# Kernel tuning notes

Hardware: AMD Instinct MI355X
Metric: run time of the kernel (lower is better)

## Reference

```python
import jax, jax.numpy as jnp
import numpy as np

N_BLOCK = 3; EMBED = 256; N_HEAD = 8; HEAD = EMBED // N_HEAD
N_AGENT = 8; SEQ = 256; BATCH = 64; ACT_DIM = 32
DECAY_SCALE = 1.0
EPS = 1e-6


def _decay_matrix():
    # Per-head decay kappas as in Mava Sable, decay over timesteps (pos // n_agent), causal mask.
    gammas = (1.0 - jnp.exp(jnp.linspace(jnp.log(1.0 / 32.0), jnp.log(1.0 / 512.0), N_HEAD))) * DECAY_SCALE
    t = (jnp.arange(SEQ) // N_AGENT).astype(jnp.float32)
    diff = t[:, None] - t[None, :]
    causal = jnp.arange(SEQ)[:, None] >= jnp.arange(SEQ)[None, :]
    return jnp.where(causal[None], gammas[:, None, None] ** diff[None], 0.0)  # [H,S,S]


def rmsnorm(x, scale):
    return x * jax.lax.rsqrt(jnp.mean(x * x, -1, keepdims=True) + EPS) * scale


def groupnorm(x, scale, bias):
    # GroupNorm with n_head groups over the feature dim, per position.
    B, S, E = x.shape
    xg = x.reshape(B, S, N_HEAD, HEAD)
    mu = xg.mean(-1, keepdims=True)
    var = ((xg - mu) ** 2).mean(-1, keepdims=True)
    xn = ((xg - mu) * jax.lax.rsqrt(var + 1e-5)).reshape(B, S, E)
    return xn * scale + bias


def retention(q_in, k_in, v_in, wq, wk, wv, wg, wo, gns, gnb, decay):
    # Parallel multi-scale retention: (Q K^T * D) V, groupnorm, swish gate from query input.
    B, S, E = q_in.shape
    q = (q_in @ wq).reshape(B, S, N_HEAD, HEAD).transpose(0, 2, 1, 3)
    k = (k_in @ wk).reshape(B, S, N_HEAD, HEAD).transpose(0, 2, 1, 3) / jnp.sqrt(jnp.float32(HEAD))
    v = (v_in @ wv).reshape(B, S, N_HEAD, HEAD).transpose(0, 2, 1, 3)
    scores = jnp.einsum('bhnd,bhmd->bhnm', q, k) * decay[None]
    ret = jnp.einsum('bhnm,bhmd->bhnd', scores, v)
    ret = groupnorm(ret.transpose(0, 2, 1, 3).reshape(B, S, E), gns, gnb)
    return (jax.nn.swish(q_in @ wg) * ret) @ wo


def swiglu(x, wg, w1, w2):
    return (jax.nn.swish(x @ wg) * (x @ w1)) @ w2


def forward(action, obs_rep, w_enc, ln0, wq1, wk1, wv1, wg1, wo1, gns1, gnb1, ln1,
            wq2, wk2, wv2, wg2, wo2, gns2, gnb2, ln2, swg, sw1, sw2, ln3,
            hw1, hb1, hln, hw2, hb2):
    decay = _decay_matrix()
    x = rmsnorm(jax.nn.gelu(action @ w_enc), ln0)
    for b in range(N_BLOCK):
        r1 = retention(x, x, x, wq1[b], wk1[b], wv1[b], wg1[b], wo1[b], gns1[b], gnb1[b], decay)
        x = rmsnorm(x + r1, ln1[b])
        r2 = retention(obs_rep, x, x, wq2[b], wk2[b], wv2[b], wg2[b], wo2[b], gns2[b], gnb2[b], decay)
        x = rmsnorm(obs_rep + r2, ln2[b])
        x = rmsnorm(x + swiglu(x, swg[b], sw1[b], sw2[b]), ln3[b])
    h = rmsnorm(jax.nn.gelu(x @ hw1 + hb1), hln)
    return h @ hw2 + hb2


def setup_inputs() -> dict:
    key = jax.random.key(0)
    ks = jax.random.split(key, 24)
    E, A, NB = EMBED, ACT_DIM, N_BLOCK
    s = 0.02
    return {
        'action': jax.random.uniform(ks[0], (BATCH, SEQ, A), jnp.float32),
        'obs_rep': jax.random.normal(ks[1], (BATCH, SEQ, E), jnp.float32),
        'w_enc': jax.random.normal(ks[2], (A, E), jnp.float32) * s,
        'ln0': jnp.ones((E,), jnp.float32),
        'wq1': jax.random.normal(ks[3], (NB, E, E), jnp.float32) * s,
        'wk1': jax.random.normal(ks[4], (NB, E, E), jnp.float32) * s,
        'wv1': jax.random.normal(ks[5], (NB, E, E), jnp.float32) * s,
        'wg1': jax.random.normal(ks[6], (NB, E, E), jnp.float32) * s,
        'wo1': jax.random.normal(ks[7], (NB, E, E), jnp.float32) * s,
        'gns1': jnp.ones((NB, E), jnp.float32),
        'gnb1': jnp.zeros((NB, E), jnp.float32),
        'ln1': jnp.ones((NB, E), jnp.float32),
        'wq2': jax.random.normal(ks[8], (NB, E, E), jnp.float32) * s,
        'wk2': jax.random.normal(ks[9], (NB, E, E), jnp.float32) * s,
        'wv2': jax.random.normal(ks[10], (NB, E, E), jnp.float32) * s,
        'wg2': jax.random.normal(ks[11], (NB, E, E), jnp.float32) * s,
        'wo2': jax.random.normal(ks[12], (NB, E, E), jnp.float32) * s,
        'gns2': jnp.ones((NB, E), jnp.float32),
        'gnb2': jnp.zeros((NB, E), jnp.float32),
        'ln2': jnp.ones((NB, E), jnp.float32),
        'swg': jax.random.normal(ks[13], (NB, E, E), jnp.float32) * s,
        'sw1': jax.random.normal(ks[14], (NB, E, E), jnp.float32) * s,
        'sw2': jax.random.normal(ks[15], (NB, E, E), jnp.float32) * s,
        'ln3': jnp.ones((NB, E), jnp.float32),
        'hw1': jax.random.normal(ks[16], (E, E), jnp.float32) * s,
        'hb1': jnp.zeros((E,), jnp.float32),
        'hln': jnp.ones((E,), jnp.float32),
        'hw2': jax.random.normal(ks[17], (E, A), jnp.float32) * s,
        'hb2': jnp.zeros((A,), jnp.float32),
    }


def reference(action, obs_rep, w_enc, ln0, wq1, wk1, wv1, wg1, wo1, gns1, gnb1, ln1,
              wq2, wk2, wv2, wg2, wo2, gns2, gnb2, ln2, swg, sw1, sw2, ln3,
              hw1, hb1, hln, hw2, hb2):
    return forward(action, obs_rep, w_enc, ln0, wq1, wk1, wv1, wg1, wo1, gns1, gnb1, ln1,
                   wq2, wk2, wv2, wg2, wo2, gns2, gnb2, ln2, swg, sw1, sw2, ln3,
                   hw1, hb1, hln, hw2, hb2)
```

## Files before the change

### kernel.cpp

```cpp
#include <hip/hip_runtime.h>
#include <cstdint>
#include <cmath>

typedef __attribute__((ext_vector_type(8))) short short8;
typedef __attribute__((ext_vector_type(4))) float floatx4;

#define DEV static __device__ __forceinline__

DEV float bf2f(uint16_t u) {
    union { uint32_t i; float f; } v; v.i = ((uint32_t)u) << 16; return v.f;
}
DEV uint16_t f2bf(float f) {
    union { float f; uint32_t i; } v; v.f = f;
    uint32_t r = (v.i + 0x7FFFu + ((v.i >> 16) & 1u)) >> 16;
    return (uint16_t)r;
}
DEV float swishf(float x) { return x / (1.f + __expf(-x)); }
DEV float geluf(float x) {
    const float c = 0.7978845608028654f;
    float t = tanhf(c * (x + 0.044715f * x * x * x));
    return 0.5f * x * (1.f + t);
}

#define CHUNK_E 8192
#define MAT_E   65536


struct TArg { const float* src[15]; };

__global__ __launch_bounds__(256) void tpose_k(TArg ta, uint16_t* __restrict__ arena) {
    int z = blockIdx.z;
    const float* src; uint16_t* dst;
    if (z == 0) {
        if (blockIdx.y) return;
        src = ta.src[0]; dst = arena;
    } else if (z <= 39) {
        int q = z - 1; int ti = q / 3, s = q % 3;
        src = ta.src[1 + ti] + (size_t)s * 65536;
        dst = arena + CHUNK_E + (size_t)(ti * 3 + s) * MAT_E;
    } else {
        src = ta.src[14]; dst = arena + CHUNK_E + (size_t)39 * MAT_E;
    }
    int k0 = blockIdx.y << 5;
    int n0 = blockIdx.x << 6;
    __shared__ __align__(16) uint16_t tile[32][72];
    int t = threadIdx.x;
    {
        int r = t >> 3, c = (t & 7) << 3;
        const float* s0 = src + (size_t)(k0 + r) * 256 + n0 + c;
        float4 f0 = *(const float4*)s0;
        float4 f1 = *(const float4*)(s0 + 4);
        tile[r][c + 0] = f2bf(f0.x); tile[r][c + 1] = f2bf(f0.y);
        tile[r][c + 2] = f2bf(f0.z); tile[r][c + 3] = f2bf(f0.w);
        tile[r][c + 4] = f2bf(f1.x); tile[r][c + 5] = f2bf(f1.y);
        tile[r][c + 6] = f2bf(f1.z); tile[r][c + 7] = f2bf(f1.w);
    }
    __syncthreads();
    {
        int n = t >> 2, c = (t & 3) << 3;
        uint16_t tmp[8];
#pragma unroll
        for (int j = 0; j < 8; ++j) tmp[j] = tile[c + j][n];
        *(uint4*)&dst[(size_t)(k0 >> 5) * CHUNK_E + (size_t)(n0 + n) * 32 + c] = *(uint4*)tmp;
    }
}

struct SegArgs {
    const float* action; const float* obs;
    uint16_t *actb, *obsb, *xb, *bq, *bk, *bv, *bg, *brg;
    const float *ln0, *hb1, *hln, *hw2, *hb2;
    float* outp;
    float l2g[8];
};

enum { EP_NONE = 0, EP_GELU_RMS = 1, EP_RESID_RMS = 2 };
enum { EP2_NONE = 0, EP2_SWIGLU = 1 };

template<int EPI, int K>
DEV void gemm_dev(int m0, const uint16_t* __restrict__ A, const uint16_t* __restrict__ Wt,
                  uint16_t* __restrict__ O, const float* __restrict__ bias,
                  const uint16_t* __restrict__ resid, const float* __restrict__ lnw,
                  float (&rowsum)[4][32])
{
    const int t = threadIdx.x;
    const int w = t >> 6, lane = t & 63, l16 = lane & 15, lg = lane >> 4;
    constexpr int NC = K / 32;

    floatx4 acc[2][4];
#pragma unroll
    for (int i = 0; i < 2; ++i)
#pragma unroll
        for (int j = 0; j < 4; ++j) acc[i][j] = (floatx4){0.f, 0.f, 0.f, 0.f};

#pragma unroll
    for (int kc = 0; kc < NC; ++kc) {
        short8 aF[2], bF[4];
#pragma unroll
        for (int rt = 0; rt < 2; ++rt)
            aF[rt] = *(const short8*)(A + (size_t)(m0 + (rt << 4) + l16) * K +
                                      (kc << 5) + (lg << 3));
#pragma unroll
        for (int ct = 0; ct < 4; ++ct)
            bF[ct] = *(const short8*)(Wt + (size_t)kc * CHUNK_E +
                                      (size_t)((w << 6) + (ct << 4) + l16) * 32 + (lg << 3));
#pragma unroll
        for (int rt = 0; rt < 2; ++rt)
#pragma unroll
            for (int ct = 0; ct < 4; ++ct)
                acc[rt][ct] = __builtin_amdgcn_mfma_f32_16x16x32_bf16(
                    aF[rt], bF[ct], acc[rt][ct], 0, 0, 0);
    }

    float v[2][4][4];
#pragma unroll
    for (int rt = 0; rt < 2; ++rt)
#pragma unroll
        for (int ct = 0; ct < 4; ++ct)
#pragma unroll
            for (int r = 0; r < 4; ++r) {
                int row = (rt << 4) + (lg << 2) + r;
                int col = (w << 6) + (ct << 4) + l16;
                size_t idx = (size_t)(m0 + row) * 256 + col;
                float x = acc[rt][ct][r];
                if (EPI == EP_GELU_RMS) { if (bias) x += bias[col]; x = geluf(x); }
                if (EPI == EP_RESID_RMS) x += bf2f(resid[idx]);
                v[rt][ct][r] = x;
            }

    if (EPI == EP_GELU_RMS || EPI == EP_RESID_RMS) {
#pragma unroll
        for (int rt = 0; rt < 2; ++rt)
#pragma unroll
            for (int r = 0; r < 4; ++r) {
                float p = 0.f;
#pragma unroll
                for (int ct = 0; ct < 4; ++ct) p += v[rt][ct][r] * v[rt][ct][r];
                p += __shfl_xor(p, 1, 64); p += __shfl_xor(p, 2, 64);
                p += __shfl_xor(p, 4, 64); p += __shfl_xor(p, 8, 64);
                int row = (rt << 4) + (lg << 2) + r;
                if (l16 == 0) rowsum[w][row] = p;
            }
        __syncthreads();
#pragma unroll
        for (int rt = 0; rt < 2; ++rt)
#pragma unroll
            for (int r = 0; r < 4; ++r) {
                int row = (rt << 4) + (lg << 2) + r;
                float tot = rowsum[0][row] + rowsum[1][row] + rowsum[2][row] + rowsum[3][row];
                float rn = rsqrtf(tot * (1.f / 256.f) + 1e-6f);
#pragma unroll
                for (int ct = 0; ct < 4; ++ct) {
                    int col = (w << 6) + (ct << 4) + l16;
                    size_t idx = (size_t)(m0 + row) * 256 + col;
                    O[idx] = f2bf(v[rt][ct][r] * rn * lnw[col]);
                }
            }
        __syncthreads();
    } else {
#pragma unroll
        for (int rt = 0; rt < 2; ++rt)
#pragma unroll
            for (int ct = 0; ct < 4; ++ct)
#pragma unroll
                for (int r = 0; r < 4; ++r) {
                    int row = (rt << 4) + (lg << 2) + r;
                    int col = (w << 6) + (ct << 4) + l16;
                    O[(size_t)(m0 + row) * 256 + col] = f2bf(v[rt][ct][r]);
                }
    }
}

template<int EPI>
DEV void gemm2_dev(int m0, const uint16_t* __restrict__ A,
                   const uint16_t* __restrict__ W1, const uint16_t* __restrict__ W2,
                   uint16_t* __restrict__ O1, uint16_t* __restrict__ O2)
{
    const int t = threadIdx.x;
    const int w = t >> 6, lane = t & 63, l16 = lane & 15, lg = lane >> 4;

    floatx4 a1[2][4], a2[2][4];
#pragma unroll
    for (int i = 0; i < 2; ++i)
#pragma unroll
        for (int j = 0; j < 4; ++j) {
            a1[i][j] = (floatx4){0.f, 0.f, 0.f, 0.f};
            a2[i][j] = (floatx4){0.f, 0.f, 0.f, 0.f};
        }

#pragma unroll
    for (int kc = 0; kc < 8; ++kc) {
        short8 aF[2], b1[4], b2[4];
#pragma unroll
        for (int rt = 0; rt < 2; ++rt)
            aF[rt] = *(const short8*)(A + (size_t)(m0 + (rt << 4) + l16) * 256 +
                                      (kc << 5) + (lg << 3));
        size_t woff = (size_t)kc * CHUNK_E + (size_t)((w << 6) + l16) * 32 + (lg << 3);
#pragma unroll
        for (int ct = 0; ct < 4; ++ct) {
            b1[ct] = *(const short8*)(W1 + woff + (size_t)(ct << 4) * 32);
            b2[ct] = *(const short8*)(W2 + woff + (size_t)(ct << 4) * 32);
        }
#pragma unroll
        for (int rt = 0; rt < 2; ++rt)
#pragma unroll
            for (int ct = 0; ct < 4; ++ct) {
                a1[rt][ct] = __builtin_amdgcn_mfma_f32_16x16x32_bf16(aF[rt], b1[ct], a1[rt][ct], 0, 0, 0);
                a2[rt][ct] = __builtin_amdgcn_mfma_f32_16x16x32_bf16(aF[rt], b2[ct], a2[rt][ct], 0, 0, 0);
            }
    }

#pragma unroll
    for (int rt = 0; rt < 2; ++rt)
#pragma unroll
        for (int ct = 0; ct < 4; ++ct)
#pragma unroll
            for (int r = 0; r < 4; ++r) {
                int row = (rt << 4) + (lg << 2) + r;
                int col = (w << 6) + (ct << 4) + l16;
                size_t idx = (size_t)(m0 + row) * 256 + col;
                if (EPI == EP2_NONE) {
                    O1[idx] = f2bf(a1[rt][ct][r]);
                    O2[idx] = f2bf(a2[rt][ct][r]);
                } else {
                    O1[idx] = f2bf(swishf(a1[rt][ct][r]) * a2[rt][ct][r]);
                }
            }
}

DEV int rowbase(int blk) { return (blk & 63) * 256 + (blk >> 6) * 32; }


__global__ __launch_bounds__(256, 2) void seg0_k(SegArgs sa, const uint16_t* __restrict__ wenc,
                                                 const uint16_t* __restrict__ wq,
                                                 const uint16_t* __restrict__ wk,
                                                 const uint16_t* __restrict__ wv,
                                                 const uint16_t* __restrict__ wg)
{
    __shared__ float rowsum[4][32];
    const int t = threadIdx.x;
    const int m0 = rowbase(blockIdx.x);
    {
        int r = t >> 3, c = (t & 7) << 2;
        float4 f = *(const float4*)(sa.action + (size_t)(m0 + r) * 32 + c);
        uint16_t tmp[4] = { f2bf(f.x), f2bf(f.y), f2bf(f.z), f2bf(f.w) };
        *(uint2*)(sa.actb + (size_t)(m0 + r) * 32 + c) = *(uint2*)tmp;
    }
    {
        const float4* ob = (const float4*)sa.obs + (size_t)m0 * 64;
        uint2* od = (uint2*)sa.obsb + (size_t)m0 * 64;
#pragma unroll
        for (int j = 0; j < 8; ++j) {
            float4 f = ob[j * 256 + t];
            uint16_t tmp[4] = { f2bf(f.x), f2bf(f.y), f2bf(f.z), f2bf(f.w) };
            od[j * 256 + t] = *(uint2*)tmp;
        }
    }
    __syncthreads();
    gemm_dev<EP_GELU_RMS, 32>(m0, sa.actb, wenc, sa.xb, nullptr, nullptr, sa.ln0, rowsum);
    gemm2_dev<EP2_NONE>(m0, sa.xb, wq, wk, sa.bq, sa.bk);
    gemm2_dev<EP2_NONE>(m0, sa.xb, wv, wg, sa.bv, sa.bg);
}

__global__ __launch_bounds__(256, 2) void attn_k(SegArgs sa, const float* __restrict__ gns,
                                                 const float* __restrict__ gnb)
{
    __shared__ __align__(16) uint16_t QS[256][40];
    __shared__ __align__(16) uint16_t Ks[256][40];
    __shared__ __align__(16) uint16_t Vt[32][264];
    const int b = blockIdx.x & 63, h = blockIdx.x >> 6;
    const float l2g = sa.l2g[h];
    const int t = threadIdx.x, w = t >> 6, lane = t & 63, l16 = lane & 15, lg = lane >> 4;
    const size_t base = ((size_t)b * 256) * 256 + (size_t)h * 32;
    const uint16_t *q = sa.bq, *kbuf = sa.bk, *vbuf = sa.bv, *g = sa.bg;
    uint16_t* out = sa.brg;

    {
        const uint4* qr = (const uint4*)(q + base + (size_t)t * 256);
        *(uint4*)&QS[t][0] = qr[0]; *(uint4*)&QS[t][8] = qr[1];
        *(uint4*)&QS[t][16] = qr[2]; *(uint4*)&QS[t][24] = qr[3];
        const uint4* kr = (const uint4*)(kbuf + base + (size_t)t * 256);
        *(uint4*)&Ks[t][0] = kr[0]; *(uint4*)&Ks[t][8] = kr[1];
        *(uint4*)&Ks[t][16] = kr[2]; *(uint4*)&Ks[t][24] = kr[3];
        union { uint4 v4[4]; uint16_t u[32]; } vv;
        const uint4* vr = (const uint4*)(vbuf + base + (size_t)t * 256);
        vv.v4[0] = vr[0]; vv.v4[1] = vr[1]; vv.v4[2] = vr[2]; vv.v4[3] = vr[3];
#pragma unroll
        for (int d = 0; d < 32; ++d) Vt[d][t] = vv.u[d];
    }
    __syncthreads();

    short8 qF[4];
#pragma unroll
    for (int rt = 0; rt < 4; ++rt)
        qF[rt] = *(const short8*)&QS[(w << 6) + (rt << 4) + l16][lg << 3];

    floatx4 racc[4][2];
#pragma unroll
    for (int i = 0; i < 4; ++i) { racc[i][0] = (floatx4){0,0,0,0}; racc[i][1] = (floatx4){0,0,0,0}; }

    const float invsq = 0.17677669529663687f;
    const int jtmax = 2 * w + 1;
    for (int jt = 0; jt <= jtmax; ++jt) {
        const int j0 = jt << 5;
        floatx4 sacc[4][2];
#pragma unroll
        for (int i = 0; i < 4; ++i) { sacc[i][0] = (floatx4){0,0,0,0}; sacc[i][1] = (floatx4){0,0,0,0}; }
        short8 kF[2];
#pragma unroll
        for (int ct = 0; ct < 2; ++ct)
            kF[ct] = *(const short8*)&Ks[j0 + (ct << 4) + l16][lg << 3];
#pragma unroll
        for (int rt = 0; rt < 4; ++rt)
#pragma unroll
            for (int ct = 0; ct < 2; ++ct)
                sacc[rt][ct] = __builtin_amdgcn_mfma_f32_16x16x32_bf16(
                    qF[rt], kF[ct], sacc[rt][ct], 0, 0, 0);
#pragma unroll
        for (int rt = 0; rt < 4; ++rt)
#pragma unroll
            for (int ct = 0; ct < 2; ++ct)
#pragma unroll
                for (int r = 0; r < 4; ++r) {
                    int row = (rt << 4) + (lg << 2) + r;
                    int i = (w << 6) + row;
                    int j = j0 + (ct << 4) + l16;
                    float svv = 0.f;
                    if (i >= j)
                        svv = sacc[rt][ct][r] * invsq *
                              exp2f((float)((i >> 3) - (j >> 3)) * l2g);
                    QS[(w << 6) + row][(ct << 4) + l16] = f2bf(svv);
                }
        short8 vF[2];
#pragma unroll
        for (int ct = 0; ct < 2; ++ct)
            vF[ct] = *(const short8*)&Vt[(ct << 4) + l16][j0 + (lg << 3)];
#pragma unroll
        for (int rt = 0; rt < 4; ++rt) {
            short8 sF = *(const short8*)&QS[(w << 6) + (rt << 4) + l16][lg << 3];
#pragma unroll
            for (int ct = 0; ct < 2; ++ct)
                racc[rt][ct] = __builtin_amdgcn_mfma_f32_16x16x32_bf16(
                    sF, vF[ct], racc[rt][ct], 0, 0, 0);
        }
    }

#pragma unroll
    for (int rt = 0; rt < 4; ++rt)
#pragma unroll
        for (int r = 0; r < 4; ++r) {
            float v0 = racc[rt][0][r], v1 = racc[rt][1][r];
            float s1 = v0 + v1, s2 = v0 * v0 + v1 * v1;
            s1 += __shfl_xor(s1, 1, 64); s2 += __shfl_xor(s2, 1, 64);
            s1 += __shfl_xor(s1, 2, 64); s2 += __shfl_xor(s2, 2, 64);
            s1 += __shfl_xor(s1, 4, 64); s2 += __shfl_xor(s2, 4, 64);
            s1 += __shfl_xor(s1, 8, 64); s2 += __shfl_xor(s2, 8, 64);
            float mu = s1 * (1.f / 32.f);
            float var = s2 * (1.f / 32.f) - mu * mu;
            float rstd = rsqrtf(var + 1e-5f);
            int srow = (w << 6) + (rt << 4) + (lg << 2) + r;
            size_t obase = ((size_t)b * 256 + srow) * 256 + (size_t)h * 32;
#pragma unroll
            for (int ct = 0; ct < 2; ++ct) {
                int d = (ct << 4) + l16;
                float x = ct ? v1 : v0;
                float y = (x - mu) * rstd * gns[h * 32 + d] + gnb[h * 32 + d];
                float gv = swishf(bf2f(g[obase + d]));
                out[obase + d] = f2bf(y * gv);
            }
        }
}

__global__ __launch_bounds__(256, 2) void g1_k(SegArgs sa,
    const uint16_t* __restrict__ wo, const float* __restrict__ ln1,
    const uint16_t* __restrict__ wq, const uint16_t* __restrict__ wk,
    const uint16_t* __restrict__ wv, const uint16_t* __restrict__ wg)
{
    __shared__ float rowsum[4][32];
    const int m0 = rowbase(blockIdx.x);
    gemm_dev<EP_RESID_RMS, 256>(m0, sa.brg, wo, sa.xb, nullptr, sa.xb, ln1, rowsum);
    gemm2_dev<EP2_NONE>(m0, sa.xb,   wk, wv, sa.bk, sa.bv);
    gemm2_dev<EP2_NONE>(m0, sa.obsb, wq, wg, sa.bq, sa.bg);
}

__global__ __launch_bounds__(256, 2) void g2_k(SegArgs sa,
    const uint16_t* __restrict__ wo, const float* __restrict__ ln2,
    const uint16_t* __restrict__ wswg, const uint16_t* __restrict__ wsw1,
    const uint16_t* __restrict__ wsw2, const float* __restrict__ ln3,
    const uint16_t* __restrict__ nwq, const uint16_t* __restrict__ nwk,
    const uint16_t* __restrict__ nwv, const uint16_t* __restrict__ nwg)
{
    __shared__ float rowsum[4][32];
    const int m0 = rowbase(blockIdx.x);
    gemm_dev<EP_RESID_RMS, 256>(m0, sa.brg, wo, sa.xb, nullptr, sa.obsb, ln2, rowsum);
    gemm2_dev<EP2_SWIGLU>(m0, sa.xb, wswg, wsw1, sa.bk, nullptr);
    __syncthreads();
    gemm_dev<EP_RESID_RMS, 256>(m0, sa.bk, wsw2, sa.xb, nullptr, sa.xb, ln3, rowsum);
    if (nwq) {
        gemm2_dev<EP2_NONE>(m0, sa.xb, nwq, nwk, sa.bq, sa.bk);
        gemm2_dev<EP2_NONE>(m0, sa.xb, nwv, nwg, sa.bv, sa.bg);
    }
}

__global__ __launch_bounds__(256, 2) void head_k(SegArgs sa, const uint16_t* __restrict__ hw1t)
{
    __shared__ float rowsum[4][32];
    __shared__ float w2s[8192];
    const int t = threadIdx.x;
    const int m0 = rowbase(blockIdx.x);
    gemm_dev<EP_GELU_RMS, 256>(m0, sa.xb, hw1t, sa.bq, sa.hb1, nullptr, sa.hln, rowsum);
    __syncthreads();
#pragma unroll
    for (int j = 0; j < 32; ++j) w2s[j * 256 + t] = sa.hw2[j * 256 + t];
    __syncthreads();
    {
        int n = t & 31, rs = t >> 5;
#pragma unroll
        for (int rr = 0; rr < 4; ++rr) {
            int row = m0 + (rr << 3) + rs;
            float a0 = sa.hb2[n];
#pragma unroll 8
            for (int kk = 0; kk < 256; ++kk)
                a0 += bf2f(sa.bq[(size_t)row * 256 + kk]) * w2s[kk * 32 + n];
            sa.outp[(size_t)row * 32 + n] = a0;
        }
    }
}

extern "C" void kernel_launch(void* const* d_in, const int* in_sizes, int n_in,
                              void* d_out, int out_size, void* d_ws, size_t ws_size,
                              hipStream_t stream)
{
    const float* action = (const float*)d_in[0];
    const float* obs    = (const float*)d_in[1];
    const float* w_enc  = (const float*)d_in[2];
    const float* ln0    = (const float*)d_in[3];
    const float* wq1 = (const float*)d_in[4];
    const float* wk1 = (const float*)d_in[5];
    const float* wv1 = (const float*)d_in[6];
    const float* wg1 = (const float*)d_in[7];
    const float* wo1 = (const float*)d_in[8];
    const float* gns1 = (const float*)d_in[9];
    const float* gnb1 = (const float*)d_in[10];
    const float* ln1  = (const float*)d_in[11];
    const float* wq2 = (const float*)d_in[12];
    const float* wk2 = (const float*)d_in[13];
    const float* wv2 = (const float*)d_in[14];
    const float* wg2 = (const float*)d_in[15];
    const float* wo2 = (const float*)d_in[16];
    const float* gns2 = (const float*)d_in[17];
    const float* gnb2 = (const float*)d_in[18];
    const float* ln2  = (const float*)d_in[19];
    const float* swgp = (const float*)d_in[20];
    const float* sw1p = (const float*)d_in[21];
    const float* sw2p = (const float*)d_in[22];
    const float* ln3  = (const float*)d_in[23];
    const float* hw1  = (const float*)d_in[24];
    const float* hb1  = (const float*)d_in[25];
    const float* hln  = (const float*)d_in[26];
    const float* hw2  = (const float*)d_in[27];
    const float* hb2  = (const float*)d_in[28];

    char* ws = (char*)d_ws;
    uint16_t* wt   = (uint16_t*)(ws + 0);
    uint16_t* actb = (uint16_t*)(ws + 6291456);
    uint16_t* obsb = (uint16_t*)(ws + 7340032);
    uint16_t* xb   = (uint16_t*)(ws + 15728640);
    uint16_t* bq   = (uint16_t*)(ws + 24117248);
    uint16_t* bk   = (uint16_t*)(ws + 32505856);
    uint16_t* bv   = (uint16_t*)(ws + 40894464);
    uint16_t* bg   = (uint16_t*)(ws + 49283072);
    uint16_t* brg  = (uint16_t*)(ws + 57671680);

    uint16_t* wtenc = wt;
    uint16_t* hw1t  = wt + CHUNK_E + (size_t)39 * MAT_E;
    auto WTp = [&](int ti, int s) { return wt + CHUNK_E + (size_t)(ti * 3 + s) * MAT_E; };

    TArg ta;
    ta.src[0] = w_enc;
    ta.src[1] = wq1;  ta.src[2] = wk1;  ta.src[3] = wv1;  ta.src[4] = wg1;  ta.src[5] = wo1;
    ta.src[6] = wq2;  ta.src[7] = wk2;  ta.src[8] = wv2;  ta.src[9] = wg2;  ta.src[10] = wo2;
    ta.src[11] = swgp; ta.src[12] = sw1p; ta.src[13] = sw2p; ta.src[14] = hw1;
    tpose_k<<<dim3(4, 8, 41), 256, 0, stream>>>(ta, wt);

    SegArgs sa;
    sa.action = action; sa.obs = obs;
    sa.actb = actb; sa.obsb = obsb; sa.xb = xb;
    sa.bq = bq; sa.bk = bk; sa.bv = bv; sa.bg = bg; sa.brg = brg;
    sa.ln0 = ln0; sa.hb1 = hb1; sa.hln = hln; sa.hw2 = hw2; sa.hb2 = hb2;
    sa.outp = (float*)d_out;
    {
        const double a = log(1.0 / 32.0), bb = log(1.0 / 512.0);
        for (int hh = 0; hh < 8; ++hh) {
            double lg = a + (bb - a) * hh / 7.0;
            double gam = 1.0 - exp(lg);
            sa.l2g[hh] = (float)(log(gam) / log(2.0));
        }
    }

    dim3 GB(512), TB(256);
    seg0_k<<<GB, TB, 0, stream>>>(sa, wtenc, WTp(0, 0), WTp(1, 0), WTp(2, 0), WTp(3, 0));
    for (int b3 = 0; b3 < 3; ++b3) {
        attn_k<<<GB, TB, 0, stream>>>(sa, gns1 + b3 * 256, gnb1 + b3 * 256);
        g1_k<<<GB, TB, 0, stream>>>(sa, WTp(4, b3), ln1 + b3 * 256,
                                    WTp(5, b3), WTp(6, b3), WTp(7, b3), WTp(8, b3));
        attn_k<<<GB, TB, 0, stream>>>(sa, gns2 + b3 * 256, gnb2 + b3 * 256);
        g2_k<<<GB, TB, 0, stream>>>(sa, WTp(9, b3), ln2 + b3 * 256,
                                    WTp(10, b3), WTp(11, b3), WTp(12, b3), ln3 + b3 * 256,
                                    b3 < 2 ? WTp(0, b3 + 1) : nullptr,
                                    b3 < 2 ? WTp(1, b3 + 1) : nullptr,
                                    b3 < 2 ? WTp(2, b3 + 1) : nullptr,
                                    b3 < 2 ? WTp(3, b3 + 1) : nullptr);
    }
    head_k<<<GB, TB, 0, stream>>>(sa, hw1t);
}
```

Baseline: 605.8 us.

## Keep intermediate row tiles in padded LDS between chained GEMMs

The fused GEMM helpers gain template options to read A from, and write outputs to, padded shared-memory tiles (row stride 264). Intermediates produced and consumed by the same block now stay in LDS rather than round-tripping through global bf16 buffers. This covers the encoder output, the post-wo residual norm, the SwiGLU hidden and the head hidden. Global stores are kept only where later kernels need them. The cost is more shared memory per block, which may reduce occupancy below the two blocks per CU that the launch bounds target, especially in g2_k and head_k.

```diff
diff --git a/kernel.cpp b/kernel.cpp
--- a/kernel.cpp
+++ b/kernel.cpp
@@ -24,6 +24,7 @@
 
 #define CHUNK_E 8192
 #define MAT_E   65536
+#define APAD    264
 
 
 struct TArg { const float* src[15]; };
@@ -76,11 +77,17 @@
 enum { EP_NONE = 0, EP_GELU_RMS = 1, EP_RESID_RMS = 2 };
 enum { EP2_NONE = 0, EP2_SWIGLU = 1 };
 
-template<int EPI, int K>
-DEV void gemm_dev(int m0, const uint16_t* __restrict__ A, const uint16_t* __restrict__ Wt,
-                  uint16_t* __restrict__ O, const float* __restrict__ bias,
-                  const uint16_t* __restrict__ resid, const float* __restrict__ lnw,
-                  float (&rowsum)[4][32])
+template<int EPI, int K, int LDA, bool OG, int LDO, bool RL>
+DEV void gemm_u(int m0,
+                const uint16_t* __restrict__ A,
+                const uint16_t* __restrict__ Wt,
+                uint16_t* __restrict__ Og,
+                uint16_t* __restrict__ Ol,
+                const float* __restrict__ bias,
+                const uint16_t* __restrict__ Rg,
+                const uint16_t* __restrict__ Rl,
+                const float* __restrict__ lnw,
+                float (&rowsum)[4][32])
 {
     const int t = threadIdx.x;
     const int w = t >> 6, lane = t & 63, l16 = lane & 15, lg = lane >> 4;
@@ -96,9 +103,13 @@
     for (int kc = 0; kc < NC; ++kc) {
         short8 aF[2], bF[4];
 #pragma unroll
-        for (int rt = 0; rt < 2; ++rt)
-            aF[rt] = *(const short8*)(A + (size_t)(m0 + (rt << 4) + l16) * K +
-                                      (kc << 5) + (lg << 3));
+        for (int rt = 0; rt < 2; ++rt) {
+            int row = (rt << 4) + l16;
+            if constexpr (LDA != 0)
+                aF[rt] = *(const short8*)(A + (size_t)row * LDA + (kc << 5) + (lg << 3));
+            else
+                aF[rt] = *(const short8*)(A + (size_t)(m0 + row) * K + (kc << 5) + (lg << 3));
+        }
 #pragma unroll
         for (int ct = 0; ct < 4; ++ct)
             bF[ct] = *(const short8*)(Wt + (size_t)kc * CHUNK_E +
@@ -120,14 +131,19 @@
             for (int r = 0; r < 4; ++r) {
                 int row = (rt << 4) + (lg << 2) + r;
                 int col = (w << 6) + (ct << 4) + l16;
-                size_t idx = (size_t)(m0 + row) * 256 + col;
                 float x = acc[rt][ct][r];
-                if (EPI == EP_GELU_RMS) { if (bias) x += bias[col]; x = geluf(x); }
-                if (EPI == EP_RESID_RMS) x += bf2f(resid[idx]);
+                if constexpr (EPI == EP_GELU_RMS) {
+                    if (bias) x += bias[col];
+                    x = geluf(x);
+                }
+                if constexpr (EPI == EP_RESID_RMS) {
+                    if constexpr (RL) x += bf2f(Rl[(size_t)row * APAD + col]);
+                    else              x += bf2f(Rg[(size_t)(m0 + row) * 256 + col]);
+                }
                 v[rt][ct][r] = x;
             }
 
-    if (EPI == EP_GELU_RMS || EPI == EP_RESID_RMS) {
+    if constexpr (EPI == EP_GELU_RMS || EPI == EP_RESID_RMS) {
 #pragma unroll
         for (int rt = 0; rt < 2; ++rt)
 #pragma unroll
@@ -151,8 +167,11 @@
 #pragma unroll
                 for (int ct = 0; ct < 4; ++ct) {
                     int col = (w << 6) + (ct << 4) + l16;
-                    size_t idx = (size_t)(m0 + row) * 256 + col;
-                    O[idx] = f2bf(v[rt][ct][r] * rn * lnw[col]);
+                    uint16_t bb = f2bf(v[rt][ct][r] * rn * lnw[col]);
+                    if constexpr (OG)
+                        Og[(size_t)(m0 + row) * 256 + col] = bb;
+                    if constexpr (LDO != 0)
+                        Ol[(size_t)row * LDO + col] = bb;
                 }
             }
         __syncthreads();
@@ -165,15 +184,20 @@
                 for (int r = 0; r < 4; ++r) {
                     int row = (rt << 4) + (lg << 2) + r;
                     int col = (w << 6) + (ct << 4) + l16;
-                    O[(size_t)(m0 + row) * 256 + col] = f2bf(v[rt][ct][r]);
+                    uint16_t bb = f2bf(v[rt][ct][r]);
+                    if constexpr (OG)
+                        Og[(size_t)(m0 + row) * 256 + col] = bb;
+                    if constexpr (LDO != 0)
+                        Ol[(size_t)row * LDO + col] = bb;
                 }
     }
 }
 
-template<int EPI>
-DEV void gemm2_dev(int m0, const uint16_t* __restrict__ A,
-                   const uint16_t* __restrict__ W1, const uint16_t* __restrict__ W2,
-                   uint16_t* __restrict__ O1, uint16_t* __restrict__ O2)
+template<int EPI, int LDA>
+DEV void gemm2_u(int m0, const uint16_t* __restrict__ A,
+                 const uint16_t* __restrict__ W1, const uint16_t* __restrict__ W2,
+                 uint16_t* __restrict__ O1, uint16_t* __restrict__ O2,
+                 uint16_t* __restrict__ Ol)
 {
     const int t = threadIdx.x;
     const int w = t >> 6, lane = t & 63, l16 = lane & 15, lg = lane >> 4;
@@ -191,9 +215,13 @@
     for (int kc = 0; kc < 8; ++kc) {
         short8 aF[2], b1[4], b2[4];
 #pragma unroll
-        for (int rt = 0; rt < 2; ++rt)
-            aF[rt] = *(const short8*)(A + (size_t)(m0 + (rt << 4) + l16) * 256 +
-                                      (kc << 5) + (lg << 3));
+        for (int rt = 0; rt < 2; ++rt) {
+            int row = (rt << 4) + l16;
+            if constexpr (LDA != 0)
+                aF[rt] = *(const short8*)(A + (size_t)row * LDA + (kc << 5) + (lg << 3));
+            else
+                aF[rt] = *(const short8*)(A + (size_t)(m0 + row) * 256 + (kc << 5) + (lg << 3));
+        }
         size_t woff = (size_t)kc * CHUNK_E + (size_t)((w << 6) + l16) * 32 + (lg << 3);
 #pragma unroll
         for (int ct = 0; ct < 4; ++ct) {
@@ -217,12 +245,12 @@
             for (int r = 0; r < 4; ++r) {
                 int row = (rt << 4) + (lg << 2) + r;
                 int col = (w << 6) + (ct << 4) + l16;
-                size_t idx = (size_t)(m0 + row) * 256 + col;
-                if (EPI == EP2_NONE) {
+                if constexpr (EPI == EP2_NONE) {
+                    size_t idx = (size_t)(m0 + row) * 256 + col;
                     O1[idx] = f2bf(a1[rt][ct][r]);
                     O2[idx] = f2bf(a2[rt][ct][r]);
                 } else {
-                    O1[idx] = f2bf(swishf(a1[rt][ct][r]) * a2[rt][ct][r]);
+                    Ol[(size_t)row * APAD + col] = f2bf(swishf(a1[rt][ct][r]) * a2[rt][ct][r]);
                 }
             }
 }
@@ -237,13 +265,15 @@
                                                  const uint16_t* __restrict__ wg)
 {
     __shared__ float rowsum[4][32];
+    __shared__ __align__(16) uint16_t actS[32][40];
+    __shared__ __align__(16) uint16_t T0[32][APAD];
     const int t = threadIdx.x;
     const int m0 = rowbase(blockIdx.x);
     {
         int r = t >> 3, c = (t & 7) << 2;
         float4 f = *(const float4*)(sa.action + (size_t)(m0 + r) * 32 + c);
         uint16_t tmp[4] = { f2bf(f.x), f2bf(f.y), f2bf(f.z), f2bf(f.w) };
-        *(uint2*)(sa.actb + (size_t)(m0 + r) * 32 + c) = *(uint2*)tmp;
+        *(uint2*)&actS[r][c] = *(uint2*)tmp;
     }
     {
         const float4* ob = (const float4*)sa.obs + (size_t)m0 * 64;
@@ -256,9 +286,10 @@
         }
     }
     __syncthreads();
-    gemm_dev<EP_GELU_RMS, 32>(m0, sa.actb, wenc, sa.xb, nullptr, nullptr, sa.ln0, rowsum);
-    gemm2_dev<EP2_NONE>(m0, sa.xb, wq, wk, sa.bq, sa.bk);
-    gemm2_dev<EP2_NONE>(m0, sa.xb, wv, wg, sa.bv, sa.bg);
+    gemm_u<EP_GELU_RMS, 32, 40, true, APAD, false>(m0, &actS[0][0], wenc,
+        sa.xb, &T0[0][0], nullptr, nullptr, nullptr, sa.ln0, rowsum);
+    gemm2_u<EP2_NONE, APAD>(m0, &T0[0][0], wq, wk, sa.bq, sa.bk, nullptr);
+    gemm2_u<EP2_NONE, APAD>(m0, &T0[0][0], wv, wg, sa.bv, sa.bg, nullptr);
 }
 
 __global__ __launch_bounds__(256, 2) void attn_k(SegArgs sa, const float* __restrict__ gns,
@@ -376,10 +407,12 @@
     const uint16_t* __restrict__ wv, const uint16_t* __restrict__ wg)
 {
     __shared__ float rowsum[4][32];
+    __shared__ __align__(16) uint16_t T0[32][APAD];
     const int m0 = rowbase(blockIdx.x);
-    gemm_dev<EP_RESID_RMS, 256>(m0, sa.brg, wo, sa.xb, nullptr, sa.xb, ln1, rowsum);
-    gemm2_dev<EP2_NONE>(m0, sa.xb,   wk, wv, sa.bk, sa.bv);
-    gemm2_dev<EP2_NONE>(m0, sa.obsb, wq, wg, sa.bq, sa.bg);
+    gemm_u<EP_RESID_RMS, 256, 0, false, APAD, false>(m0, sa.brg, wo,
+        nullptr, &T0[0][0], nullptr, sa.xb, nullptr, ln1, rowsum);
+    gemm2_u<EP2_NONE, APAD>(m0, &T0[0][0], wk, wv, sa.bk, sa.bv, nullptr);
+    gemm2_u<EP2_NONE, 0>(m0, sa.obsb, wq, wg, sa.bq, sa.bg, nullptr);
 }
 
 __global__ __launch_bounds__(256, 2) void g2_k(SegArgs sa,
@@ -390,14 +423,18 @@
     const uint16_t* __restrict__ nwv, const uint16_t* __restrict__ nwg)
 {
     __shared__ float rowsum[4][32];
+    __shared__ __align__(16) uint16_t T0[32][APAD];
+    __shared__ __align__(16) uint16_t T1[32][APAD];
     const int m0 = rowbase(blockIdx.x);
-    gemm_dev<EP_RESID_RMS, 256>(m0, sa.brg, wo, sa.xb, nullptr, sa.obsb, ln2, rowsum);
-    gemm2_dev<EP2_SWIGLU>(m0, sa.xb, wswg, wsw1, sa.bk, nullptr);
+    gemm_u<EP_RESID_RMS, 256, 0, false, APAD, false>(m0, sa.brg, wo,
+        nullptr, &T0[0][0], nullptr, sa.obsb, nullptr, ln2, rowsum);
+    gemm2_u<EP2_SWIGLU, APAD>(m0, &T0[0][0], wswg, wsw1, nullptr, nullptr, &T1[0][0]);
     __syncthreads();
-    gemm_dev<EP_RESID_RMS, 256>(m0, sa.bk, wsw2, sa.xb, nullptr, sa.xb, ln3, rowsum);
+    gemm_u<EP_RESID_RMS, 256, APAD, true, APAD, true>(m0, &T1[0][0], wsw2,
+        sa.xb, &T0[0][0], nullptr, nullptr, &T0[0][0], ln3, rowsum);
     if (nwq) {
-        gemm2_dev<EP2_NONE>(m0, sa.xb, nwq, nwk, sa.bq, sa.bk);
-        gemm2_dev<EP2_NONE>(m0, sa.xb, nwv, nwg, sa.bv, sa.bg);
+        gemm2_u<EP2_NONE, APAD>(m0, &T0[0][0], nwq, nwk, sa.bq, sa.bk, nullptr);
+        gemm2_u<EP2_NONE, APAD>(m0, &T0[0][0], nwv, nwg, sa.bv, sa.bg, nullptr);
     }
 }
 
@@ -405,23 +442,23 @@
 {
     __shared__ float rowsum[4][32];
     __shared__ float w2s[8192];
+    __shared__ __align__(16) uint16_t T0[32][APAD];
     const int t = threadIdx.x;
     const int m0 = rowbase(blockIdx.x);
-    gemm_dev<EP_GELU_RMS, 256>(m0, sa.xb, hw1t, sa.bq, sa.hb1, nullptr, sa.hln, rowsum);
-    __syncthreads();
 #pragma unroll
     for (int j = 0; j < 32; ++j) w2s[j * 256 + t] = sa.hw2[j * 256 + t];
-    __syncthreads();
+    gemm_u<EP_GELU_RMS, 256, 0, false, APAD, false>(m0, sa.xb, hw1t,
+        nullptr, &T0[0][0], sa.hb1, nullptr, nullptr, sa.hln, rowsum);
     {
         int n = t & 31, rs = t >> 5;
 #pragma unroll
         for (int rr = 0; rr < 4; ++rr) {
-            int row = m0 + (rr << 3) + rs;
+            int lrow = (rr << 3) + rs;
             float a0 = sa.hb2[n];
 #pragma unroll 8
             for (int kk = 0; kk < 256; ++kk)
-                a0 += bf2f(sa.bq[(size_t)row * 256 + kk]) * w2s[kk * 32 + n];
-            sa.outp[(size_t)row * 32 + n] = a0;
+                a0 += bf2f(T0[lrow][kk]) * w2s[kk * 32 + n];
+            sa.outp[(size_t)(m0 + lrow) * 32 + n] = a0;
         }
     }
 }
```

Result: no change. 606.8 us (+0.2%).
